# Kernel optimization log

Measured on AMD Instinct MI355X. Metric: run time of the kernel, lower is better.

## Reference

```python
import jax, jax.numpy as jnp
import numpy as np

B, NPG, DEG = 32, 1024, 16          # graphs, nodes/graph, avg degree
N, E = B * NPG, B * NPG * DEG        # 32768 nodes, 524288 edges
IN_C, HID, H, EDGE_D = 128, 64, 4, 8
RATIO = 0.5
K = int(np.ceil(RATIO * NPG))        # 512 nodes kept per graph (static)
SLOPE = 0.2                          # PyG GATConv LeakyReLU default


def setup_inputs() -> dict:
    key = jax.random.key(0)
    ks = jax.random.split(key, 10)
    x = jax.random.normal(ks[0], (N, IN_C), jnp.float32)
    # edges confined within each graph (block structure like PyG Batch)
    src_l = jax.random.randint(ks[1], (B, NPG * DEG), 0, NPG)
    dst_l = jax.random.randint(ks[2], (B, NPG * DEG), 0, NPG)
    off = (jnp.arange(B) * NPG)[:, None]
    edge_index = jnp.stack([(src_l + off).reshape(-1), (dst_l + off).reshape(-1)]).astype(jnp.int64)
    edge = jax.random.normal(ks[3], (E, EDGE_D), jnp.float32)
    batch_index = jnp.repeat(jnp.arange(B), NPG).astype(jnp.int64)
    s_in = 1.0 / np.sqrt(IN_C)
    W = jax.random.normal(ks[4], (IN_C, H, HID), jnp.float32) * s_in
    a_src = jax.random.normal(ks[5], (H, HID), jnp.float32) * s_in
    a_dst = jax.random.normal(ks[6], (H, HID), jnp.float32) * s_in
    b_gat = jnp.zeros((H * HID,), jnp.float32)
    W_lin = jax.random.normal(ks[7], (H * HID, HID), jnp.float32) * (1.0 / np.sqrt(H * HID))
    b_lin = jnp.zeros((HID,), jnp.float32)
    p_pool = jax.random.normal(ks[8], (HID,), jnp.float32)
    return dict(x=x, edge_index=edge_index, edge=edge, batch_index=batch_index,
                W=W, a_src=a_src, a_dst=a_dst, b_gat=b_gat,
                W_lin=W_lin, b_lin=b_lin, p_pool=p_pool)


def reference(x, edge_index, edge, batch_index, W, a_src, a_dst, b_gat, W_lin, b_lin, p_pool):
    n = x.shape[0]
    # --- GATConv (heads concat, self-loops added, softmax over incoming edges) ---
    loops = jnp.arange(n)
    src = jnp.concatenate([edge_index[0], loops])
    dst = jnp.concatenate([edge_index[1], loops])
    h = jnp.einsum('ni,ihc->nhc', x, W)                  # [N,H,C]
    al_src = (h * a_src).sum(-1)                          # [N,H]
    al_dst = (h * a_dst).sum(-1)                          # [N,H]
    e = jax.nn.leaky_relu(al_src[src] + al_dst[dst], SLOPE)  # [Etot,H]
    m = jax.ops.segment_max(e, dst, num_segments=n)
    ex = jnp.exp(e - m[dst])
    denom = jax.ops.segment_sum(ex, dst, num_segments=n)
    alpha = ex / denom[dst]                               # segment softmax per target
    out = jax.ops.segment_sum(h[src] * alpha[:, :, None], dst, num_segments=n)
    xg = out.reshape(n, H * HID) + b_gat
    # --- Linear ---
    xl = xg @ W_lin + b_lin                               # [N,HID]
    # --- TopKPooling (tanh(x.p/||p||) score, top ceil(ratio*n) per graph) ---
    score = jnp.tanh(xl @ p_pool / jnp.linalg.norm(p_pool))   # [N]
    topv, topi = jax.lax.top_k(score.reshape(B, NPG), K)      # [B,K]
    perm = (topi + (jnp.arange(B) * NPG)[:, None]).reshape(-1)  # global kept node ids
    xp = xl[perm] * topv.reshape(-1)[:, None]             # [B*K,HID], gated by score
    batch_out = jnp.repeat(jnp.arange(B), K)
    # edge filtering / remapping (padded with -1 instead of compacting)
    nmap = jnp.full((n,), -1, jnp.int32).at[perm].set(jnp.arange(B * K, dtype=jnp.int32))
    ns, nd = nmap[edge_index[0]], nmap[edge_index[1]]
    valid = (ns >= 0) & (nd >= 0)
    edge_index_new = jnp.where(valid, jnp.stack([ns, nd]), -1)
    edge_new = jnp.where(valid[:, None], edge, 0.0)
    # --- global mean/max pool (graphs are contiguous blocks of K nodes) ---
    xr = xp.reshape(B, K, HID)
    x1 = jnp.concatenate([xr.mean(axis=1), xr.max(axis=1)], axis=-1)  # [B,2*HID]
    return xp, edge_index_new, edge_new, batch_out, x1
```

## Files before the change

kernel.cpp:

```cpp
#include <hip/hip_runtime.h>
#include <math.h>

#define NN   32768
#define EE   524288
#define ETOT (EE + NN)
#define BB   32
#define NPG  1024
#define EPG  16384
#define RPG  17408
#define KK   512
#define INC  128
#define HID  64
#define NH   4
#define CC   256
#define SLOPE 0.2f

typedef __attribute__((ext_vector_type(8))) short short8;
typedef __attribute__((ext_vector_type(4))) float f32x4;

static __device__ inline unsigned short f2bf(float f) {
  unsigned u = __float_as_uint(f);
  unsigned r = (u + 0x7FFFu + ((u >> 16) & 1u)) >> 16;
  return (unsigned short)r;
}

static __device__ inline void atomicMaxF(float* addr, float value) {
  if (!(__float_as_uint(value) >> 31)) {
    atomicMax((int*)addr, __float_as_int(value));
  } else {
    atomicMin((unsigned int*)addr, __float_as_uint(value));
  }
}

__global__ __launch_bounds__(1024) void prep_kernel(const float* __restrict__ W,
                                                    const float* __restrict__ a_src,
                                                    const float* __restrict__ a_dst,
                                                    const float* __restrict__ b_gat,
                                                    const float* __restrict__ W_lin,
                                                    const float* __restrict__ b_lin,
                                                    const float* __restrict__ p,
                                                    float* __restrict__ Mg,
                                                    float* __restrict__ cbuf,
                                                    unsigned short* __restrict__ Wt,
                                                    unsigned short* __restrict__ Wlt,
                                                    const int* __restrict__ ei,
                                                    int* __restrict__ row_ptr,
                                                    int* __restrict__ col) {
  const int b = blockIdx.x, t = threadIdx.x;
  if (b >= 65) {
    __shared__ int hist[NPG];
    __shared__ int lpos[NPG];
    __shared__ int wsum[16];
    const int bb = b - 65;
    const int lane = t & 63, wid = t >> 6;
    hist[t] = 0;
    __syncthreads();
    const int e0 = bb * EPG;
    for (int k = t; k < EPG; k += 1024)
      atomicAdd(&hist[ei[EE + e0 + k] - bb * NPG], 1);
    __syncthreads();
    const int c = hist[t] + 1;
    int inc = c;
#pragma unroll
    for (int off = 1; off < 64; off <<= 1) {
      int u = __shfl_up(inc, off, 64);
      if (lane >= off) inc += u;
    }
    if (lane == 63) wsum[wid] = inc;
    __syncthreads();
    if (wid == 0) {
      int v = (lane < 16) ? wsum[lane] : 0;
#pragma unroll
      for (int off = 1; off < 16; off <<= 1) {
        int u = __shfl_up(v, off, 64);
        if (lane >= off) v += u;
      }
      if (lane < 16) wsum[lane] = v;
    }
    __syncthreads();
    const int woff = (wid == 0) ? 0 : wsum[wid - 1];
    const int excl = woff + inc - c;
    row_ptr[bb * NPG + t] = bb * RPG + excl;
    lpos[t] = excl;
    if (bb == 0 && t == 0) row_ptr[NN] = ETOT;
    __syncthreads();
    {
      int p0 = atomicAdd(&lpos[t], 1);
      col[bb * RPG + p0] = bb * NPG + t;
    }
    for (int k = t; k < EPG; k += 1024) {
      int s = ei[e0 + k];
      int d = ei[EE + e0 + k];
      int p1 = atomicAdd(&lpos[d - bb * NPG], 1);
      col[bb * RPG + p1] = s;
    }
    return;
  }
  if (b >= 17) {
    int idx = (b - 17) * 1024 + t;
    if (idx < 32768) {
      int c = idx >> 7, k = idx & 127;
      Wt[idx] = f2bf(W[k * 256 + c]);
    } else {
      int i2 = idx - 32768;
      int c = i2 >> 8, k = i2 & 255;
      Wlt[i2] = f2bf(W_lin[k * 64 + c]);
    }
    return;
  }
  __shared__ float pl[64];
  __shared__ float ql[256];
  __shared__ float red[256];
  __shared__ float red2[256];
  if (t < 64) pl[t] = p[t];
  __syncthreads();
  if (t < 256) {
    float acc = 0.f;
    const float* wr = W_lin + t * 64;
#pragma unroll
    for (int c = 0; c < 64; c += 4) {
      float4 wv = *(const float4*)(wr + c);
      acc += wv.x * pl[c] + wv.y * pl[c + 1] + wv.z * pl[c + 2] + wv.w * pl[c + 3];
    }
    ql[t] = acc;
  }
  __syncthreads();
  if (b == 0) {
    if (t < 256) {
      float r = ql[t] * b_gat[t];
      if (t < 64) r += b_lin[t] * pl[t];
      red[t] = r;
      red2[t] = (t < 64) ? pl[t] * pl[t] : 0.f;
    }
    __syncthreads();
    for (int s2 = 128; s2 > 0; s2 >>= 1) {
      if (t < s2) { red[t] += red[t + s2]; red2[t] += red2[t + s2]; }
      __syncthreads();
    }
    if (t == 0) { cbuf[0] = red[0]; cbuf[1] = 1.0f / sqrtf(red2[0]); }
    return;
  }
  if (t < 96) {
    const int i = (b - 1) * 8 + t / 12;
    const int j = t % 12;
    const int hh = j & 3;
    const float* wr = W + i * 256 + hh * 64;
    float acc = 0.f;
    if (j < 8) {
      const float* v = (j < 4 ? a_src : a_dst) + hh * 64;
#pragma unroll
      for (int c = 0; c < 64; c += 4) {
        float4 wv = *(const float4*)(wr + c);
        float4 vv = *(const float4*)(v + c);
        acc += wv.x * vv.x + wv.y * vv.y + wv.z * vv.z + wv.w * vv.w;
      }
    } else {
#pragma unroll
      for (int c = 0; c < 64; ++c) acc += wr[c] * ql[hh * 64 + c];
    }
    Mg[i * 12 + j] = acc;
  }
}

__global__ __launch_bounds__(256) void stage2_kernel(const float* __restrict__ x,
                                                     const float* __restrict__ Mg,
                                                     const unsigned short* __restrict__ Wt,
                                                     float* __restrict__ al_s,
                                                     float* __restrict__ al_d,
                                                     float* __restrict__ hq,
                                                     unsigned short* __restrict__ hbf) {
  __shared__ float smem[76 * 132];
  const int t = threadIdx.x;
  if (blockIdx.x >= 512) {
    float (*xs)[132] = (float(*)[132])smem;
    float (*MsT)[132] = (float(*)[132])(smem + 64 * 132);
    const int n0 = (blockIdx.x - 512) * 64;
    for (int r = t; r < 1536; r += 256) MsT[r % 12][r / 12] = Mg[r];
#pragma unroll
    for (int u = 0; u < 8; ++u) {
      int idx = u * 256 + t;
      int node = idx >> 5, c4 = idx & 31;
      *(float4*)(&xs[node][c4 * 4]) =
          *(const float4*)(x + (size_t)(n0 + node) * 128 + c4 * 4);
    }
    __syncthreads();
    const int node = t >> 2, q = t & 3;
    const int j0 = q * 3;
    float a0 = 0.f, a1 = 0.f, a2 = 0.f;
#pragma unroll
    for (int c4 = 0; c4 < 32; ++c4) {
      float4 xv = *(const float4*)(&xs[node][c4 * 4]);
      float4 m0 = *(const float4*)(&MsT[j0 + 0][c4 * 4]);
      float4 m1 = *(const float4*)(&MsT[j0 + 1][c4 * 4]);
      float4 m2 = *(const float4*)(&MsT[j0 + 2][c4 * 4]);
      a0 += xv.x * m0.x + xv.y * m0.y + xv.z * m0.z + xv.w * m0.w;
      a1 += xv.x * m1.x + xv.y * m1.y + xv.z * m1.z + xv.w * m1.w;
      a2 += xv.x * m2.x + xv.y * m2.y + xv.z * m2.z + xv.w * m2.w;
    }
    const int n = n0 + node;
    float vals[3] = {a0, a1, a2};
#pragma unroll
    for (int k = 0; k < 3; ++k) {
      int j = j0 + k;
      float* base = (j < 4) ? al_s : ((j < 8) ? al_d : hq);
      int jj = (j < 4) ? j : ((j < 8) ? j - 4 : j - 8);
      base[n * 4 + jj] = vals[k];
    }
    return;
  }
  const int lane = t & 63;
  const int wv = t >> 6;
  const int q = lane >> 4, nh = lane & 15;
  const int lid = blockIdx.x;
  const int node = ((lid & 7) * 64 + (lid >> 3)) * 64 + wv * 16 + nh;
  f32x4 acc[16];
#pragma unroll
  for (int mt = 0; mt < 16; ++mt) acc[mt] = (f32x4){0.f, 0.f, 0.f, 0.f};
  const float* xr = x + (size_t)node * 128;
#pragma unroll
  for (int kc = 0; kc < 4; ++kc) {
    const float* xp = xr + kc * 32 + q * 8;
    float4 v0 = *(const float4*)(xp);
    float4 v1 = *(const float4*)(xp + 4);
    short8 b;
    b[0] = (short)f2bf(v0.x); b[1] = (short)f2bf(v0.y);
    b[2] = (short)f2bf(v0.z); b[3] = (short)f2bf(v0.w);
    b[4] = (short)f2bf(v1.x); b[5] = (short)f2bf(v1.y);
    b[6] = (short)f2bf(v1.z); b[7] = (short)f2bf(v1.w);
#pragma unroll
    for (int mt = 0; mt < 16; ++mt) {
      short8 a = *(const short8*)(Wt + (size_t)(mt * 16 + nh) * 128 + kc * 32 + q * 8);
      acc[mt] = __builtin_amdgcn_mfma_f32_16x16x32_bf16(a, b, acc[mt], 0, 0, 0);
    }
  }
  unsigned short* hr = hbf + (size_t)node * 256;
#pragma unroll
  for (int mt = 0; mt < 16; ++mt) {
    ushort4 o;
    o.x = f2bf(acc[mt][0]); o.y = f2bf(acc[mt][1]);
    o.z = f2bf(acc[mt][2]); o.w = f2bf(acc[mt][3]);
    *(ushort4*)(hr + mt * 16 + q * 4) = o;
  }
}

__global__ __launch_bounds__(256) void agg_kernel(const unsigned short* __restrict__ h,
                                                  const float* __restrict__ al_s,
                                                  const float* __restrict__ al_d,
                                                  const float* __restrict__ hq,
                                                  const int* __restrict__ row_ptr,
                                                  const int* __restrict__ col,
                                                  const float* __restrict__ b_gat,
                                                  const float* __restrict__ cbuf,
                                                  unsigned short* __restrict__ outg,
                                                  float* __restrict__ score) {
  __shared__ float wsh[4][256];
  __shared__ float qsh[4][256];
  __shared__ int   osh[4][64];
  const int lane = threadIdx.x & 63;
  const int wv = threadIdx.x >> 6;
  const int hqi = lane >> 4;
  const int xcd = blockIdx.x & 7;
  const int jb = blockIdx.x >> 3;
  const int n = (xcd * 1024 + jb) * 4 + wv;
  const int beg = row_ptr[n], end = row_ptr[n + 1];
  const float4 ad4 = *(const float4*)(al_d + (size_t)n * 4);
  const char* hbase = (const char*)h + (size_t)lane * 8;
  float ax = 0.f, ay = 0.f, az = 0.f, aw = 0.f, den = 0.f, sq = 0.f;
  for (int base = beg; base < end; base += 64) {
    const int rem = end - base;
    const int cnt = rem < 64 ? rem : 64;
    if (lane < cnt) {
      const int c = col[base + lane];
      osh[wv][lane] = c << 9;
      const float4 as = *(const float4*)(al_s + (size_t)c * 4);
      float e0 = as.x + ad4.x; e0 = (e0 > 0.f) ? e0 : SLOPE * e0;
      float e1 = as.y + ad4.y; e1 = (e1 > 0.f) ? e1 : SLOPE * e1;
      float e2 = as.z + ad4.z; e2 = (e2 > 0.f) ? e2 : SLOPE * e2;
      float e3 = as.w + ad4.w; e3 = (e3 > 0.f) ? e3 : SLOPE * e3;
      *(float4*)(&wsh[wv][lane * 4]) =
          make_float4(__expf(e0), __expf(e1), __expf(e2), __expf(e3));
      *(float4*)(&qsh[wv][lane * 4]) = *(const float4*)(hq + (size_t)c * 4);
    }
    const int cm1 = cnt - 1;
    uint2 v0 = *(const uint2*)(hbase + osh[wv][0]);
    uint2 v1 = *(const uint2*)(hbase + osh[wv][1 > cm1 ? cm1 : 1]);
    uint2 v2 = *(const uint2*)(hbase + osh[wv][2 > cm1 ? cm1 : 2]);
    uint2 v3 = *(const uint2*)(hbase + osh[wv][3 > cm1 ? cm1 : 3]);
    for (int i = 0; i < cnt; ++i) {
      const float w = wsh[wv][i * 4 + hqi];
      const float hqv = qsh[wv][i * 4 + hqi];
      uint2 cur = v0; v0 = v1; v1 = v2; v2 = v3;
      int ni = i + 4; ni = ni > cm1 ? cm1 : ni;
      v3 = *(const uint2*)(hbase + osh[wv][ni]);
      den += w; sq += w * hqv;
      ax += w * __uint_as_float(cur.x << 16);
      ay += w * __uint_as_float(cur.x & 0xffff0000u);
      az += w * __uint_as_float(cur.y << 16);
      aw += w * __uint_as_float(cur.y & 0xffff0000u);
    }
  }
  const float4 bg = *(const float4*)(b_gat + lane * 4);
  ushort4 ov;
  ov.x = f2bf(ax / den + bg.x); ov.y = f2bf(ay / den + bg.y);
  ov.z = f2bf(az / den + bg.z); ov.w = f2bf(aw / den + bg.w);
  *(ushort4*)(outg + (size_t)n * 256 + lane * 4) = ov;
  float sd = sq / den;
  float s0v = __shfl(sd, 0), s1v = __shfl(sd, 16);
  float s2v = __shfl(sd, 32), s3v = __shfl(sd, 48);
  if (lane == 0)
    score[n] = tanhf((s0v + s1v + s2v + s3v + cbuf[0]) * cbuf[1]);
}

__global__ __launch_bounds__(1024) void topk_kernel(const float* __restrict__ score,
                                                    int* __restrict__ pidx_g,
                                                    float* __restrict__ tvs_g,
                                                    int* __restrict__ nmap,
                                                    float* __restrict__ out_batch,
                                                    float* __restrict__ out_x1) {
  __shared__ float scv[NPG];
  const int blk = blockIdx.x;
  const int b = blk >> 3, slice = blk & 7;
  const int t = threadIdx.x;
  if (slice == 0 && t < 128)
    out_x1[b * 128 + t] = (t < 64) ? 0.f : -INFINITY;
  scv[t] = score[b * NPG + t];
  __syncthreads();
  const int node = slice * 128 + (t >> 3);
  const int sub = t & 7;
  const float sc = scv[node];
  int rank = 0;
#pragma unroll
  for (int m = 0; m < 32; ++m) {
    const int j = (m * 8 + sub) * 4;
    const float4 s4 = *(const float4*)(&scv[j]);
    rank += (s4.x > sc) || (s4.x == sc && (j + 0) < node);
    rank += (s4.y > sc) || (s4.y == sc && (j + 1) < node);
    rank += (s4.z > sc) || (s4.z == sc && (j + 2) < node);
    rank += (s4.w > sc) || (s4.w == sc && (j + 3) < node);
  }
  rank += __shfl_xor(rank, 1, 64);
  rank += __shfl_xor(rank, 2, 64);
  rank += __shfl_xor(rank, 4, 64);
  if (sub == 0) {
    const int gn = b * NPG + node;
    if (rank < KK) {
      pidx_g[b * KK + rank] = node;
      tvs_g[b * KK + rank] = sc;
      nmap[gn] = b * KK + rank;
      out_batch[b * KK + rank] = (float)b;
    } else {
      nmap[gn] = -1;
    }
  }
}

__global__ __launch_bounds__(256) void final_kernel(const unsigned short* __restrict__ outg,
                                                    const unsigned short* __restrict__ Wlt,
                                                    const float* __restrict__ bl,
                                                    const int* __restrict__ pidx_g,
                                                    const float* __restrict__ tvs_g,
                                                    const int* __restrict__ ei,
                                                    const float* __restrict__ edge,
                                                    const int* __restrict__ nmap,
                                                    float* __restrict__ out_xp,
                                                    float* __restrict__ out_ei,
                                                    float* __restrict__ out_edge,
                                                    float* __restrict__ out_x1) {
  __shared__ float tile[64][68];
  __shared__ float pr[4][64];
  __shared__ float pmx[4][64];
  const int t = threadIdx.x;
  if (blockIdx.x >= 256) {
    int e = (blockIdx.x - 256) * 256 + t;
    int s = ei[e], d = ei[EE + e];
    int ns = nmap[s], nd = nmap[d];
    bool valid = (ns >= 0) && (nd >= 0);
    out_ei[e] = (float)(valid ? ns : -1);
    out_ei[EE + e] = (float)(valid ? nd : -1);
    const float4* ef = (const float4*)(edge + (size_t)e * 8);
    float4 z = make_float4(0.f, 0.f, 0.f, 0.f);
    float4 v0 = valid ? ef[0] : z;
    float4 v1 = valid ? ef[1] : z;
    float4* eo = (float4*)(out_edge + (size_t)e * 8);
    eo[0] = v0; eo[1] = v1;
    return;
  }
  const int lane = t & 63, wv = t >> 6;
  const int q = lane >> 4, nh = lane & 15;
  const int g = blockIdx.x >> 3, o = blockIdx.x & 7;
  const int r = o * 64 + wv * 16 + nh;
  const int row = wv * 16 + nh;
  const int gnode = g * NPG + pidx_g[g * KK + r];
  const float tv = tvs_g[g * KK + r];
  f32x4 acc[4];
#pragma unroll
  for (int mt = 0; mt < 4; ++mt) acc[mt] = (f32x4){0.f, 0.f, 0.f, 0.f};
  const unsigned short* ar = outg + (size_t)gnode * 256;
#pragma unroll
  for (int kc = 0; kc < 8; ++kc) {
    short8 bf = *(const short8*)(ar + kc * 32 + q * 8);
#pragma unroll
    for (int mt = 0; mt < 4; ++mt) {
      short8 a = *(const short8*)(Wlt + (size_t)(mt * 16 + nh) * 256 + kc * 32 + q * 8);
      acc[mt] = __builtin_amdgcn_mfma_f32_16x16x32_bf16(a, bf, acc[mt], 0, 0, 0);
    }
  }
#pragma unroll
  for (int mt = 0; mt < 4; ++mt) {
    const int c4 = mt * 16 + q * 4;
    float4 bl4 = *(const float4*)(bl + c4);
    float4 o4 = make_float4((acc[mt][0] + bl4.x) * tv, (acc[mt][1] + bl4.y) * tv,
                            (acc[mt][2] + bl4.z) * tv, (acc[mt][3] + bl4.w) * tv);
    *(float4*)(out_xp + (size_t)(g * KK + r) * HID + c4) = o4;
    *(float4*)(&tile[row][c4]) = o4;
  }
  __syncthreads();
  {
    const int ch = t & 63, qr = t >> 6;
    float s = 0.f, m = -INFINITY;
#pragma unroll
    for (int rr = 0; rr < 16; ++rr) {
      float v = tile[qr * 16 + rr][ch];
      s += v; m = fmaxf(m, v);
    }
    pr[qr][ch] = s; pmx[qr][ch] = m;
  }
  __syncthreads();
  if (t < 64) {
    float s = pr[0][t] + pr[1][t] + pr[2][t] + pr[3][t];
    float m = fmaxf(fmaxf(pmx[0][t], pmx[1][t]), fmaxf(pmx[2][t], pmx[3][t]));
    atomicAdd(&out_x1[g * 128 + t], s * (1.0f / KK));
    atomicMaxF(&out_x1[g * 128 + 64 + t], m);
  }
}

extern "C" void kernel_launch(void* const* d_in, const int* in_sizes, int n_in,
                              void* d_out, int out_size, void* d_ws, size_t ws_size,
                              hipStream_t stream) {
  const float* x      = (const float*)d_in[0];
  const int*   ei     = (const int*)d_in[1];
  const float* edge   = (const float*)d_in[2];
  const float* W      = (const float*)d_in[4];
  const float* a_src  = (const float*)d_in[5];
  const float* a_dst  = (const float*)d_in[6];
  const float* b_gat  = (const float*)d_in[7];
  const float* W_lin  = (const float*)d_in[8];
  const float* b_lin  = (const float*)d_in[9];
  const float* p_pool = (const float*)d_in[10];

  char* ws = (char*)d_ws;
  size_t off = 0;
  auto alloc = [&](size_t bytes) -> void* {
    void* p = ws + off;
    off += (bytes + 255) & ~(size_t)255;
    return p;
  };
  unsigned short* hbf  = (unsigned short*)alloc((size_t)NN * CC * 2);
  unsigned short* outg = (unsigned short*)alloc((size_t)NN * CC * 2);
  float* al_s    = (float*)alloc((size_t)NN * NH * 4);
  float* al_d    = (float*)alloc((size_t)NN * NH * 4);
  float* hq      = (float*)alloc((size_t)NN * NH * 4);
  float* score   = (float*)alloc((size_t)NN * 4);
  int*   row_ptr = (int*)alloc((size_t)(NN + 1) * 4);
  int*   col     = (int*)alloc((size_t)ETOT * 4);
  int*   nmap    = (int*)alloc((size_t)NN * 4);
  int*   pidx_g  = (int*)alloc((size_t)BB * KK * 4);
  float* tvs_g   = (float*)alloc((size_t)BB * KK * 4);
  unsigned short* Wt  = (unsigned short*)alloc((size_t)CC * INC * 2);
  unsigned short* Wlt = (unsigned short*)alloc((size_t)HID * CC * 2);
  float* Mg      = (float*)alloc((size_t)INC * 12 * 4);
  float* cbuf    = (float*)alloc(2 * 4);

  float* out_xp    = (float*)d_out;
  float* out_ei    = out_xp + (size_t)BB * KK * HID;
  float* out_edge  = out_ei + 2 * (size_t)EE;
  float* out_batch = out_edge + (size_t)EE * 8;
  float* out_x1    = out_batch + (size_t)BB * KK;

  prep_kernel<<<97, 1024, 0, stream>>>(W, a_src, a_dst, b_gat, W_lin, b_lin,
                                       p_pool, Mg, cbuf, Wt, Wlt, ei, row_ptr, col);
  stage2_kernel<<<1024, 256, 0, stream>>>(x, Mg, Wt, al_s, al_d, hq, hbf);
  agg_kernel<<<NN / 4, 256, 0, stream>>>(hbf, al_s, al_d, hq, row_ptr, col,
                                         b_gat, cbuf, outg, score);
  topk_kernel<<<256, 1024, 0, stream>>>(score, pidx_g, tvs_g, nmap, out_batch,
                                        out_x1);
  final_kernel<<<2304, 256, 0, stream>>>(outg, Wlt, b_lin, pidx_g, tvs_g,
                                         ei, edge, nmap, out_xp, out_ei,
                                         out_edge, out_x1);
}
```

Before: 199.7 us.

## Restructure attention-logit blocks to one node per thread; batch gathers in aggregation

The attention-logit half of stage2 now gives each thread one node. It reads its x row straight from global memory and computes all 12 projections in registers, instead of staging 64 nodes of x in shared memory. This cuts that half from 512 to 128 blocks, drops the shared-memory staging, and writes results as float4. The aggregation loop now loads 8 neighbour rows per step with padded zero-weight entries instead of a 4-deep rolling prefetch with clamping, so more gathers are in flight at once. The risks are uncoalesced per-thread row reads of x and higher register pressure from 12 accumulators plus 8 outstanding loads.

```diff
diff --git a/kernel.cpp b/kernel.cpp
--- a/kernel.cpp
+++ b/kernel.cpp
@@ -169,43 +169,27 @@
                                                      float* __restrict__ al_d,
                                                      float* __restrict__ hq,
                                                      unsigned short* __restrict__ hbf) {
-  __shared__ float smem[76 * 132];
+  __shared__ float MsT[12][132];
   const int t = threadIdx.x;
   if (blockIdx.x >= 512) {
-    float (*xs)[132] = (float(*)[132])smem;
-    float (*MsT)[132] = (float(*)[132])(smem + 64 * 132);
-    const int n0 = (blockIdx.x - 512) * 64;
     for (int r = t; r < 1536; r += 256) MsT[r % 12][r / 12] = Mg[r];
-#pragma unroll
-    for (int u = 0; u < 8; ++u) {
-      int idx = u * 256 + t;
-      int node = idx >> 5, c4 = idx & 31;
-      *(float4*)(&xs[node][c4 * 4]) =
-          *(const float4*)(x + (size_t)(n0 + node) * 128 + c4 * 4);
-    }
-    __syncthreads();
-    const int node = t >> 2, q = t & 3;
-    const int j0 = q * 3;
-    float a0 = 0.f, a1 = 0.f, a2 = 0.f;
-#pragma unroll
+    __syncthreads();
+    const int n = (blockIdx.x - 512) * 256 + t;
+    float acc[12];
+#pragma unroll
+    for (int j = 0; j < 12; ++j) acc[j] = 0.f;
+    const float* xr = x + (size_t)n * 128;
     for (int c4 = 0; c4 < 32; ++c4) {
-      float4 xv = *(const float4*)(&xs[node][c4 * 4]);
-      float4 m0 = *(const float4*)(&MsT[j0 + 0][c4 * 4]);
-      float4 m1 = *(const float4*)(&MsT[j0 + 1][c4 * 4]);
-      float4 m2 = *(const float4*)(&MsT[j0 + 2][c4 * 4]);
-      a0 += xv.x * m0.x + xv.y * m0.y + xv.z * m0.z + xv.w * m0.w;
-      a1 += xv.x * m1.x + xv.y * m1.y + xv.z * m1.z + xv.w * m1.w;
-      a2 += xv.x * m2.x + xv.y * m2.y + xv.z * m2.z + xv.w * m2.w;
-    }
-    const int n = n0 + node;
-    float vals[3] = {a0, a1, a2};
-#pragma unroll
-    for (int k = 0; k < 3; ++k) {
-      int j = j0 + k;
-      float* base = (j < 4) ? al_s : ((j < 8) ? al_d : hq);
-      int jj = (j < 4) ? j : ((j < 8) ? j - 4 : j - 8);
-      base[n * 4 + jj] = vals[k];
-    }
+      const float4 xv = *(const float4*)(xr + c4 * 4);
+#pragma unroll
+      for (int j = 0; j < 12; ++j) {
+        const float4 m = *(const float4*)(&MsT[j][c4 * 4]);
+        acc[j] += xv.x * m.x + xv.y * m.y + xv.z * m.z + xv.w * m.w;
+      }
+    }
+    *(float4*)(al_s + (size_t)n * 4) = make_float4(acc[0], acc[1], acc[2], acc[3]);
+    *(float4*)(al_d + (size_t)n * 4) = make_float4(acc[4], acc[5], acc[6], acc[7]);
+    *(float4*)(hq + (size_t)n * 4) = make_float4(acc[8], acc[9], acc[10], acc[11]);
     return;
   }
   const int lane = t & 63;
@@ -269,34 +253,38 @@
   for (int base = beg; base < end; base += 64) {
     const int rem = end - base;
     const int cnt = rem < 64 ? rem : 64;
-    if (lane < cnt) {
-      const int c = col[base + lane];
+    {
+      int cl = base + lane;
+      if (cl >= end) cl = end - 1;
+      const int c = col[cl];
       osh[wv][lane] = c << 9;
       const float4 as = *(const float4*)(al_s + (size_t)c * 4);
       float e0 = as.x + ad4.x; e0 = (e0 > 0.f) ? e0 : SLOPE * e0;
       float e1 = as.y + ad4.y; e1 = (e1 > 0.f) ? e1 : SLOPE * e1;
       float e2 = as.z + ad4.z; e2 = (e2 > 0.f) ? e2 : SLOPE * e2;
       float e3 = as.w + ad4.w; e3 = (e3 > 0.f) ? e3 : SLOPE * e3;
+      const float valid = (lane < cnt) ? 1.f : 0.f;
       *(float4*)(&wsh[wv][lane * 4]) =
-          make_float4(__expf(e0), __expf(e1), __expf(e2), __expf(e3));
+          make_float4(__expf(e0) * valid, __expf(e1) * valid,
+                      __expf(e2) * valid, __expf(e3) * valid);
       *(float4*)(&qsh[wv][lane * 4]) = *(const float4*)(hq + (size_t)c * 4);
     }
-    const int cm1 = cnt - 1;
-    uint2 v0 = *(const uint2*)(hbase + osh[wv][0]);
-    uint2 v1 = *(const uint2*)(hbase + osh[wv][1 > cm1 ? cm1 : 1]);
-    uint2 v2 = *(const uint2*)(hbase + osh[wv][2 > cm1 ? cm1 : 2]);
-    uint2 v3 = *(const uint2*)(hbase + osh[wv][3 > cm1 ? cm1 : 3]);
-    for (int i = 0; i < cnt; ++i) {
-      const float w = wsh[wv][i * 4 + hqi];
-      const float hqv = qsh[wv][i * 4 + hqi];
-      uint2 cur = v0; v0 = v1; v1 = v2; v2 = v3;
-      int ni = i + 4; ni = ni > cm1 ? cm1 : ni;
-      v3 = *(const uint2*)(hbase + osh[wv][ni]);
-      den += w; sq += w * hqv;
-      ax += w * __uint_as_float(cur.x << 16);
-      ay += w * __uint_as_float(cur.x & 0xffff0000u);
-      az += w * __uint_as_float(cur.y << 16);
-      aw += w * __uint_as_float(cur.y & 0xffff0000u);
+    const int cntr = (cnt + 7) & ~7;
+    for (int i = 0; i < cntr; i += 8) {
+      uint2 vv[8];
+#pragma unroll
+      for (int k = 0; k < 8; ++k)
+        vv[k] = *(const uint2*)(hbase + osh[wv][i + k]);
+#pragma unroll
+      for (int k = 0; k < 8; ++k) {
+        const float w = wsh[wv][(i + k) * 4 + hqi];
+        const float hqv = qsh[wv][(i + k) * 4 + hqi];
+        den += w; sq += w * hqv;
+        ax += w * __uint_as_float(vv[k].x << 16);
+        ay += w * __uint_as_float(vv[k].x & 0xffff0000u);
+        az += w * __uint_as_float(vv[k].y << 16);
+        aw += w * __uint_as_float(vv[k].y & 0xffff0000u);
+      }
     }
   }
   const float4 bg = *(const float4*)(b_gat + lane * 4);
@@ -479,7 +467,7 @@
 
   prep_kernel<<<97, 1024, 0, stream>>>(W, a_src, a_dst, b_gat, W_lin, b_lin,
                                        p_pool, Mg, cbuf, Wt, Wlt, ei, row_ptr, col);
-  stage2_kernel<<<1024, 256, 0, stream>>>(x, Mg, Wt, al_s, al_d, hq, hbf);
+  stage2_kernel<<<640, 256, 0, stream>>>(x, Mg, Wt, al_s, al_d, hq, hbf);
   agg_kernel<<<NN / 4, 256, 0, stream>>>(hbf, al_s, al_d, hq, row_ptr, col,
                                          b_gat, cbuf, outg, score);
   topk_kernel<<<256, 1024, 0, stream>>>(score, pidx_g, tvs_g, nmap, out_batch,
```

Result: slower. 210.3 us (+5.3%).
